# Kernel optimization log

Hardware: AMD Instinct MI355X
Metric: run time of the kernel (lower is better)

The kernel has to match this reference:

```python
import jax, jax.numpy as jnp
import numpy as np

IN_FEATURES = 4096
OUT_FEATURES = 11008
GROUP_SIZE = 128
NBITS = 4
ALPHA = 0.05  # relative noise scale: sigma = ALPHA * |w|


def setup_inputs() -> dict:
    key = jax.random.key(0)
    k_x, k_q, k_s, k_z, k_b, k_n = jax.random.split(key, 6)
    n_groups = IN_FEATURES // GROUP_SIZE  # 32
    x = jax.random.normal(k_x, (4096, IN_FEATURES), dtype=jnp.float32)
    qweight = jax.random.randint(k_q, (OUT_FEATURES, IN_FEATURES), 0, 2 ** NBITS, dtype=jnp.int32)
    scales = jax.random.uniform(k_s, (OUT_FEATURES, n_groups), dtype=jnp.float32) * 0.01 + 1e-4
    zeros = jax.random.uniform(k_z, (OUT_FEATURES, n_groups), dtype=jnp.float32) * (2 ** NBITS)
    bias = jax.random.normal(k_b, (OUT_FEATURES,), dtype=jnp.float32)
    noise = jax.random.normal(k_n, (OUT_FEATURES, IN_FEATURES), dtype=jnp.float32)
    return {"x": x, "qweight": qweight, "scales": scales, "zeros": zeros, "bias": bias, "noise": noise}


def _dequantize(qweight, scales, zeros):
    # grouped dequant: w[o, g*G + j] = (q - zero[o,g]) * scale[o,g]
    out_f, in_f = qweight.shape
    n_groups = scales.shape[1]
    qg = qweight.reshape(out_f, n_groups, GROUP_SIZE).astype(scales.dtype)
    w = (qg - zeros[:, :, None]) * scales[:, :, None]
    return w.reshape(out_f, in_f)


def reference(x, qweight, scales, zeros, bias, noise):
    w = _dequantize(qweight, scales, zeros)[:, :IN_FEATURES]
    sigma = ALPHA * jnp.abs(w)            # noise_fn(weight, alpha)
    w_noisy = (w + noise * sigma).astype(x.dtype)
    # F.linear: x @ w.T + bias
    return jnp.einsum('bi,oi->bo', x, w_noisy) + bias
```

## Files before the change

kernel.cpp:

```cpp
#include <hip/hip_runtime.h>
#include <hip/hip_bf16.h>
#include <stdint.h>

#define M_ROWS 4096
#define IN_F   4096
#define OUT_F  11008
#define N_GROUPS 32
#define ALPHA  0.05f

typedef __bf16 bf16;
typedef __bf16 bf16x8 __attribute__((ext_vector_type(8)));
typedef float  floatx4 __attribute__((ext_vector_type(4)));

__device__ __forceinline__ void async_copy16(const void* g, void* l) {
  __builtin_amdgcn_global_load_lds(
      (const __attribute__((address_space(1))) void*)g,
      (__attribute__((address_space(3))) void*)l, 16, 0, 0);
}

__global__ __launch_bounds__(256) void prep_kernel(
    const float* __restrict__ x, const int* __restrict__ q,
    const float* __restrict__ scales, const float* __restrict__ zeros,
    const float* __restrict__ noise, bf16* __restrict__ wn,
    bf16* __restrict__ xb) {
  const int W_CH = OUT_F * (IN_F >> 3);
  const int T_CH = W_CH + (M_ROWS * (IN_F >> 3));
  const int stride = gridDim.x * 256;
  for (int idx = blockIdx.x * 256 + threadIdx.x; idx < T_CH; idx += stride) {
    if (idx < W_CH) {
      int o = idx >> 9;
      int i = (idx & 511) << 3;
      int g = i >> 7;
      float s = scales[o * N_GROUPS + g];
      float z = zeros[o * N_GROUPS + g];
      size_t base = (size_t)o * IN_F + i;
      int4   q0 = *(const int4*)(q + base);
      int4   q1 = *(const int4*)(q + base + 4);
      float4 n0 = *(const float4*)(noise + base);
      float4 n1 = *(const float4*)(noise + base + 4);
      float qs[8] = {(float)q0.x, (float)q0.y, (float)q0.z, (float)q0.w,
                     (float)q1.x, (float)q1.y, (float)q1.z, (float)q1.w};
      float ns[8] = {n0.x, n0.y, n0.z, n0.w, n1.x, n1.y, n1.z, n1.w};
      bf16x8 outv;
#pragma unroll
      for (int j = 0; j < 8; ++j) {
        float w = (qs[j] - z) * s;
        float v = fmaf(ALPHA * fabsf(w), ns[j], w);
        outv[j] = (bf16)v;
      }
      *(bf16x8*)(wn + base) = outv;
    } else {
      size_t base = (size_t)(idx - W_CH) << 3;
      float4 a0 = *(const float4*)(x + base);
      float4 a1 = *(const float4*)(x + base + 4);
      float vs[8] = {a0.x, a0.y, a0.z, a0.w, a1.x, a1.y, a1.z, a1.w};
      bf16x8 outv;
#pragma unroll
      for (int j = 0; j < 8; ++j) outv[j] = (bf16)vs[j];
      *(bf16x8*)(xb + base) = outv;
    }
  }
}

__global__ __launch_bounds__(512, 2) void gemm_8ph_kernel(
    const bf16* __restrict__ A,
    const bf16* __restrict__ W,
    const float* __restrict__ bias,
    float* __restrict__ C) {
  __shared__ bf16 lds[4 * 16384];

  const int tid = threadIdx.x;
  const int wv = tid >> 6;
  const int ln = tid & 63;
  const int wr = wv >> 2;
  const int wc = wv & 3;

  const int orig = blockIdx.x;
  const int idx  = orig >> 3;
  const int bm   = ((orig & 7) << 1) | (idx & 1);
  const int bn   = idx >> 1;
  const int mbase = bm << 8;
  const int nbase = bn << 8;

  const int dec    = (ln & 7) ^ (ln >> 3);
  const int rstage = wv * 32 + (ln >> 3) * 2 + (dec >> 2);
  const int kcol   = (dec & 3) * 8;
  const bf16* aS = A + (size_t)(mbase + rstage) * IN_F + kcol;
  const bf16* bS = W + (size_t)(nbase + rstage) * IN_F + kcol;

  const int frow = ln & 15;
  const int g4   = ln >> 4;
  const int pc   = (((frow & 1) << 2) | g4) ^ (frow >> 1);
  const int aoff =        (wr * 64 + (frow >> 1)) * 64 + pc * 8;
  const int boff = 8192 + (wc * 32 + (frow >> 1)) * 64 + pc * 8;

  floatx4 acc[8][4] = {};

#define STAGE_A(DST, KH)                                                          \
  do {                                                                            \
    async_copy16(aS + (size_t)(KH) * 32,             &lds[(DST) * 16384 + wv * 1024]);        \
    async_copy16(aS + (size_t)(KH) * 32 + 16 * IN_F, &lds[(DST) * 16384 + wv * 1024 + 512]);  \
  } while (0)
#define STAGE_B(DST, KH)                                                          \
  do {                                                                            \
    async_copy16(bS + (size_t)(KH) * 32,             &lds[(DST) * 16384 + 8192 + wv * 1024]);       \
    async_copy16(bS + (size_t)(KH) * 32 + 16 * IN_F, &lds[(DST) * 16384 + 8192 + wv * 1024 + 512]); \
  } while (0)

  STAGE_A(0, 0); STAGE_B(0, 0);
  STAGE_A(1, 1); STAGE_B(1, 1);
  STAGE_A(2, 2); STAGE_B(2, 2);
  asm volatile("s_waitcnt vmcnt(8)" ::: "memory");
  __builtin_amdgcn_s_barrier();
  __builtin_amdgcn_sched_barrier(0);

#define PAIR(SLOT, KH, DO_STAGE, TVM)                                             \
  {                                                                               \
    bf16x8 afr[4], bfr[4], afr2[4];                                               \
    _Pragma("unroll") for (int mi = 0; mi < 4; ++mi)                              \
      afr[mi] = *(const bf16x8*)&lds[(SLOT) * 16384 + aoff + mi * 512];           \
    _Pragma("unroll") for (int ni = 0; ni < 4; ++ni)                              \
      bfr[ni] = *(const bf16x8*)&lds[(SLOT) * 16384 + boff + ni * 512];           \
    if (DO_STAGE) STAGE_A(((SLOT) + 3) & 3, (KH) + 3);                            \
    __builtin_amdgcn_s_setprio(1);                                                \
    _Pragma("unroll") for (int mi = 0; mi < 4; ++mi)                              \
      _Pragma("unroll") for (int ni = 0; ni < 4; ++ni)                            \
        acc[mi][ni] = __builtin_amdgcn_mfma_f32_16x16x32_bf16(                    \
            afr[mi], bfr[ni], acc[mi][ni], 0, 0, 0);                              \
    __builtin_amdgcn_s_setprio(0);                                                \
    _Pragma("unroll") for (int mi = 0; mi < 4; ++mi)                              \
      afr2[mi] = *(const bf16x8*)&lds[(SLOT) * 16384 + aoff + (4 + mi) * 512];    \
    if (DO_STAGE) STAGE_B(((SLOT) + 3) & 3, (KH) + 3);                            \
    __builtin_amdgcn_s_setprio(1);                                                \
    _Pragma("unroll") for (int mi = 0; mi < 4; ++mi)                              \
      _Pragma("unroll") for (int ni = 0; ni < 4; ++ni)                            \
        acc[4 + mi][ni] = __builtin_amdgcn_mfma_f32_16x16x32_bf16(                \
            afr2[mi], bfr[ni], acc[4 + mi][ni], 0, 0, 0);                         \
    __builtin_amdgcn_s_setprio(0);                                                \
    asm volatile("s_waitcnt " TVM ::: "memory");                                  \
    __builtin_amdgcn_s_barrier();                                                 \
    __builtin_amdgcn_sched_barrier(0);                                            \
  }

  for (int kh = 0; kh < 124; kh += 4) {
    PAIR(0, kh + 0, true, "vmcnt(8)");
    PAIR(1, kh + 1, true, "vmcnt(8)");
    PAIR(2, kh + 2, true, "vmcnt(8)");
    PAIR(3, kh + 3, true, "vmcnt(8)");
  }
  PAIR(0, 124, true,  "vmcnt(8)");
  PAIR(1, 125, false, "vmcnt(4)");
  PAIR(2, 126, false, "vmcnt(0)");
  PAIR(3, 127, false, "vmcnt(0)");

#undef PAIR
#undef STAGE_A
#undef STAGE_B

#pragma unroll
  for (int ni = 0; ni < 4; ++ni) {
    int n = nbase + wc * 64 + ni * 16 + (ln & 15);
    float bv = bias[n];
#pragma unroll
    for (int mi = 0; mi < 8; ++mi) {
      int m0 = mbase + wr * 128 + mi * 16 + (ln >> 4) * 4;
#pragma unroll
      for (int r = 0; r < 4; ++r)
        C[(size_t)(m0 + r) * OUT_F + n] = acc[mi][ni][r] + bv;
    }
  }
}

extern "C" void kernel_launch(void* const* d_in, const int* in_sizes, int n_in,
                              void* d_out, int out_size, void* d_ws, size_t ws_size,
                              hipStream_t stream) {
  const float* x       = (const float*)d_in[0];
  const int*   qweight = (const int*)d_in[1];
  const float* scales  = (const float*)d_in[2];
  const float* zeros   = (const float*)d_in[3];
  const float* bias    = (const float*)d_in[4];
  const float* noise   = (const float*)d_in[5];
  float* out = (float*)d_out;

  bf16* wn = (bf16*)d_ws;
  bf16* xb = (bf16*)((char*)d_ws + (size_t)OUT_F * IN_F * sizeof(bf16));

  prep_kernel<<<2048, 256, 0, stream>>>(x, qweight, scales, zeros, noise, wn, xb);

  gemm_8ph_kernel<<<dim3(688), 512, 0, stream>>>(xb, wn, bias, out);
}
```

Before: 781.3 us.

## Load B fragments directly from global into registers, staging only A in LDS

Weight (B) fragments are no longer staged through LDS. Each wave now reads its own B fragments straight from global memory into registers, double-buffered across k-steps, and only A goes through the async LDS pipeline, which halves LDS use. The goal is to cut LDS traffic and shared-memory footprint. The trade-off is that B tiles shared by the waves with the same column index are fetched redundantly from global/L2, and the explicit vmcnt waits were dropped. Correctness then relies on compiler-inserted waits, including for the async LDS copies, which looks risky.

```diff
diff --git a/kernel.cpp b/kernel.cpp
--- a/kernel.cpp
+++ b/kernel.cpp
@@ -62,12 +62,12 @@
   }
 }
 
-__global__ __launch_bounds__(512, 2) void gemm_8ph_kernel(
+__global__ __launch_bounds__(512, 2) void gemm_bd_kernel(
     const bf16* __restrict__ A,
     const bf16* __restrict__ W,
     const float* __restrict__ bias,
     float* __restrict__ C) {
-  __shared__ bf16 lds[4 * 16384];
+  __shared__ bf16 lds[4 * 8192];
 
   const int tid = threadIdx.x;
   const int wv = tid >> 6;
@@ -86,76 +86,68 @@
   const int rstage = wv * 32 + (ln >> 3) * 2 + (dec >> 2);
   const int kcol   = (dec & 3) * 8;
   const bf16* aS = A + (size_t)(mbase + rstage) * IN_F + kcol;
-  const bf16* bS = W + (size_t)(nbase + rstage) * IN_F + kcol;
 
   const int frow = ln & 15;
   const int g4   = ln >> 4;
   const int pc   = (((frow & 1) << 2) | g4) ^ (frow >> 1);
-  const int aoff =        (wr * 64 + (frow >> 1)) * 64 + pc * 8;
-  const int boff = 8192 + (wc * 32 + (frow >> 1)) * 64 + pc * 8;
+  const int aoff = (wr * 64 + (frow >> 1)) * 64 + pc * 8;
+
+  const bf16* bP[4];
+#pragma unroll
+  for (int ni = 0; ni < 4; ++ni)
+    bP[ni] = W + (size_t)(nbase + wc * 64 + ni * 16 + frow) * IN_F + g4 * 8;
 
   floatx4 acc[8][4] = {};
+  bf16x8 bqA[4], bqB[4];
 
 #define STAGE_A(DST, KH)                                                          \
   do {                                                                            \
-    async_copy16(aS + (size_t)(KH) * 32,             &lds[(DST) * 16384 + wv * 1024]);        \
-    async_copy16(aS + (size_t)(KH) * 32 + 16 * IN_F, &lds[(DST) * 16384 + wv * 1024 + 512]);  \
-  } while (0)
-#define STAGE_B(DST, KH)                                                          \
-  do {                                                                            \
-    async_copy16(bS + (size_t)(KH) * 32,             &lds[(DST) * 16384 + 8192 + wv * 1024]);       \
-    async_copy16(bS + (size_t)(KH) * 32 + 16 * IN_F, &lds[(DST) * 16384 + 8192 + wv * 1024 + 512]); \
+    async_copy16(aS + (size_t)(KH) * 32,             &lds[(DST) * 8192 + wv * 1024]);        \
+    async_copy16(aS + (size_t)(KH) * 32 + 16 * IN_F, &lds[(DST) * 8192 + wv * 1024 + 512]);  \
   } while (0)
 
-  STAGE_A(0, 0); STAGE_B(0, 0);
-  STAGE_A(1, 1); STAGE_B(1, 1);
-  STAGE_A(2, 2); STAGE_B(2, 2);
-  asm volatile("s_waitcnt vmcnt(8)" ::: "memory");
+#pragma unroll
+  for (int ni = 0; ni < 4; ++ni) bqA[ni] = *(const bf16x8*)(bP[ni]);
+  STAGE_A(0, 0);
+  STAGE_A(1, 1);
+  STAGE_A(2, 2);
+  asm volatile("s_waitcnt vmcnt(4)" ::: "memory");
   __builtin_amdgcn_s_barrier();
   __builtin_amdgcn_sched_barrier(0);
 
-#define PAIR(SLOT, KH, DO_STAGE, TVM)                                             \
+#define PAIR(SLOT, KH, BQC, BQN, DO_B, DO_STAGE)                                  \
   {                                                                               \
-    bf16x8 afr[4], bfr[4], afr2[4];                                               \
-    _Pragma("unroll") for (int mi = 0; mi < 4; ++mi)                              \
-      afr[mi] = *(const bf16x8*)&lds[(SLOT) * 16384 + aoff + mi * 512];           \
-    _Pragma("unroll") for (int ni = 0; ni < 4; ++ni)                              \
-      bfr[ni] = *(const bf16x8*)&lds[(SLOT) * 16384 + boff + ni * 512];           \
+    bf16x8 afr[8];                                                                \
+    _Pragma("unroll") for (int mi = 0; mi < 8; ++mi)                              \
+      afr[mi] = *(const bf16x8*)&lds[(SLOT) * 8192 + aoff + mi * 512];            \
+    if (DO_B) {                                                                   \
+      _Pragma("unroll") for (int ni = 0; ni < 4; ++ni)                            \
+        BQN[ni] = *(const bf16x8*)(bP[ni] + ((KH) + 1) * 32);                     \
+    }                                                                             \
     if (DO_STAGE) STAGE_A(((SLOT) + 3) & 3, (KH) + 3);                            \
     __builtin_amdgcn_s_setprio(1);                                                \
-    _Pragma("unroll") for (int mi = 0; mi < 4; ++mi)                              \
+    _Pragma("unroll") for (int mi = 0; mi < 8; ++mi)                              \
       _Pragma("unroll") for (int ni = 0; ni < 4; ++ni)                            \
         acc[mi][ni] = __builtin_amdgcn_mfma_f32_16x16x32_bf16(                    \
-            afr[mi], bfr[ni], acc[mi][ni], 0, 0, 0);                              \
+            afr[mi], BQC[ni], acc[mi][ni], 0, 0, 0);                              \
     __builtin_amdgcn_s_setprio(0);                                                \
-    _Pragma("unroll") for (int mi = 0; mi < 4; ++mi)                              \
-      afr2[mi] = *(const bf16x8*)&lds[(SLOT) * 16384 + aoff + (4 + mi) * 512];    \
-    if (DO_STAGE) STAGE_B(((SLOT) + 3) & 3, (KH) + 3);                            \
-    __builtin_amdgcn_s_setprio(1);                                                \
-    _Pragma("unroll") for (int mi = 0; mi < 4; ++mi)                              \
-      _Pragma("unroll") for (int ni = 0; ni < 4; ++ni)                            \
-        acc[4 + mi][ni] = __builtin_amdgcn_mfma_f32_16x16x32_bf16(                \
-            afr2[mi], bfr[ni], acc[4 + mi][ni], 0, 0, 0);                         \
-    __builtin_amdgcn_s_setprio(0);                                                \
-    asm volatile("s_waitcnt " TVM ::: "memory");                                  \
     __builtin_amdgcn_s_barrier();                                                 \
     __builtin_amdgcn_sched_barrier(0);                                            \
   }
 
   for (int kh = 0; kh < 124; kh += 4) {
-    PAIR(0, kh + 0, true, "vmcnt(8)");
-    PAIR(1, kh + 1, true, "vmcnt(8)");
-    PAIR(2, kh + 2, true, "vmcnt(8)");
-    PAIR(3, kh + 3, true, "vmcnt(8)");
+    PAIR(0, kh + 0, bqA, bqB, true, true);
+    PAIR(1, kh + 1, bqB, bqA, true, true);
+    PAIR(2, kh + 2, bqA, bqB, true, true);
+    PAIR(3, kh + 3, bqB, bqA, true, true);
   }
-  PAIR(0, 124, true,  "vmcnt(8)");
-  PAIR(1, 125, false, "vmcnt(4)");
-  PAIR(2, 126, false, "vmcnt(0)");
-  PAIR(3, 127, false, "vmcnt(0)");
+  PAIR(0, 124, bqA, bqB, true, true);
+  PAIR(1, 125, bqB, bqA, true, false);
+  PAIR(2, 126, bqA, bqB, true, false);
+  PAIR(3, 127, bqB, bqA, false, false);
 
 #undef PAIR
 #undef STAGE_A
-#undef STAGE_B
 
 #pragma unroll
   for (int ni = 0; ni < 4; ++ni) {
@@ -187,5 +179,5 @@
 
   prep_kernel<<<2048, 256, 0, stream>>>(x, qweight, scales, zeros, noise, wn, xb);
 
-  gemm_8ph_kernel<<<dim3(688), 512, 0, stream>>>(xb, wn, bias, out);
+  gemm_bd_kernel<<<dim3(688), 512, 0, stream>>>(xb, wn, bias, out);
 }
```

Result: slower. 1.005 ms (+28.7%).
